# Performance work log

Hardware: AMD Instinct MI355X
Metric: run time of the kernel (lower is better)

Reference implementation:

```python
import jax, jax.numpy as jnp
import numpy as np

B = 1024       # batch of graphs
NUM = 512      # predicates / nodes per graph
D = 64         # embedding_dim
H = 64         # hidden_dim
E = 4096       # edges per graph (shared structure across batch)
MAIN_NUM = 10  # softmax segment [0, MAIN_NUM); sigmoid on the rest


def setup_inputs() -> dict:
    key = jax.random.key(0)
    ks = jax.random.split(key, 8)
    x = jax.random.uniform(ks[0], (B, NUM), dtype=jnp.float32)
    embedding = jax.random.normal(ks[1], (NUM, D), dtype=jnp.float32) * 0.1
    W1 = jax.random.normal(ks[2], (D, H), dtype=jnp.float32) * (1.0 / np.sqrt(D))
    b1 = jnp.zeros((H,), jnp.float32)
    W2 = jax.random.normal(ks[3], (H, H), dtype=jnp.float32) * (1.0 / np.sqrt(H))
    b2 = jnp.zeros((H,), jnp.float32)
    W3 = jax.random.normal(ks[4], (H, 1), dtype=jnp.float32) * (1.0 / np.sqrt(H))
    b3 = jnp.zeros((1,), jnp.float32)
    edge_row = jax.random.randint(ks[5], (E,), 0, NUM, dtype=jnp.int32)
    edge_col = jax.random.randint(ks[6], (E,), 0, NUM, dtype=jnp.int32)
    return {"x": x, "embedding": embedding, "W1": W1, "b1": b1,
            "W2": W2, "b2": b2, "W3": W3, "b3": b3,
            "edge_row": edge_row, "edge_col": edge_col}


def _gcn_layer(h, W, b, row, col, norm):
    # h: [B, NUM, in]; GCNConv = linear -> D^{-1/2} A D^{-1/2} aggregate -> +bias
    hW = jnp.einsum('bni,io->bno', h, W)                 # [B, NUM, out]
    msg = hW[:, row, :] * norm[None, :, None]            # [B, E, out]
    agg = jnp.zeros_like(hW).at[:, col, :].add(msg)      # scatter to targets
    return agg + b


def reference(x, embedding, W1, b1, W2, b2, W3, b3, edge_row, edge_col):
    num = x.shape[1]
    # symmetric GCN normalization (add_self_loops=False, unit edge weights)
    deg = jnp.zeros((num,), x.dtype).at[edge_col].add(1.0)
    dinv = jnp.where(deg > 0, jax.lax.rsqrt(jnp.maximum(deg, 1.0)), 0.0)
    norm = dinv[edge_row] * dinv[edge_col]               # [E]

    h = x[..., None] * embedding                         # [B, NUM, D]
    h = jax.nn.relu(_gcn_layer(h, W1, b1, edge_row, edge_col, norm))
    h = jax.nn.relu(_gcn_layer(h, W2, b2, edge_row, edge_col, norm))
    logits = _gcn_layer(h, W3, b3, edge_row, edge_col, norm)[..., 0]  # [B, NUM]

    # convert_to_confidence: softmax over multiclass segment, sigmoid elsewhere
    phi_sm = jax.nn.softmax(logits[:, :MAIN_NUM], axis=1)
    phi_sg = jax.nn.sigmoid(logits[:, MAIN_NUM:])
    return jnp.concatenate([phi_sm, phi_sg], axis=1)
```

## Files before the change

### kernel.cpp

```cpp
#include <hip/hip_runtime.h>
#include <stdint.h>

#define NB    1024
#define NUM   512
#define HD    64
#define NE    4096
#define NEP   4608
#define MAIN  10
#define HBS   72

typedef _Float16 hlf;
typedef __attribute__((ext_vector_type(2))) _Float16 hlf2;
typedef __attribute__((ext_vector_type(8))) _Float16 hlf8;
typedef __attribute__((ext_vector_type(4))) float f32x4;

__device__ __forceinline__ unsigned short f2h(float f) {
    hlf v = (hlf)f;
    return __builtin_bit_cast(unsigned short, v);
}

__global__ __launch_bounds__(512) void prep_all(
    const int* __restrict__ erow, const int* __restrict__ ecol,
    const float* __restrict__ emb, const float* __restrict__ W1,
    const float* __restrict__ W2,
    int* __restrict__ rsptr, int* __restrict__ colmap, int* __restrict__ epk,
    short* __restrict__ E1, short* __restrict__ W2T)
{
    const int t = threadIdx.x;
    if (blockIdx.x != 0) {
        int g = (blockIdx.x - 1) * 512 + t;
        if (g < NUM * HD) {
            int node = g >> 6, dim = g & 63;
            float acc = 0.0f;
            #pragma unroll
            for (int k = 0; k < HD; ++k) acc += emb[node * HD + k] * W1[k * HD + dim];
            E1[g] = (short)f2h(acc);
        } else if (g < NUM * HD + HD * HD) {
            int j = g - NUM * HD;
            int dout = j >> 6, din = j & 63;
            W2T[j] = (short)f2h(W2[din * HD + dout]);
        }
        return;
    }

    __shared__ int   sdeg[NUM];
    __shared__ int   aux[NUM];
    __shared__ float sdv[NUM];
    __shared__ int   rnk[NUM];
    __shared__ int   rdg[NUM];
    __shared__ int   wsum[8];

    const int lane = t & 63, wv = t >> 6;

    sdeg[t] = 0; aux[t] = 0;
    __syncthreads();
    for (int e = t; e < NE; e += 512) atomicAdd(&sdeg[ecol[e]], 1);
    __syncthreads();
    const int deg  = sdeg[t];
    const int pdeg = (deg + 1) & ~1;
    const int dbin = deg < NUM ? deg : NUM - 1;
    sdv[t] = deg > 0 ? rsqrtf((float)deg) : 0.0f;
    atomicAdd(&aux[dbin], 1);
    __syncthreads();
    {
        int v = aux[t];
        #pragma unroll
        for (int ofs = 1; ofs < 64; ofs <<= 1) {
            int sh = __shfl_up(v, ofs, 64);
            if (lane >= ofs) v += sh;
        }
        if (lane == 63) wsum[wv] = v;
        __syncthreads();
        if (t == 0) {
            int s = 0;
            #pragma unroll
            for (int w = 0; w < 8; ++w) { int tmp = wsum[w]; wsum[w] = s; s += tmp; }
        }
        __syncthreads();
        int inc = v + wsum[wv];
        aux[t]  = inc;
        __syncthreads();
        sdeg[t] = (t == 0) ? 0 : aux[t - 1];
        __syncthreads();
    }
    {
        int r = atomicAdd(&sdeg[dbin], 1);
        rnk[t] = r;
        rdg[r] = pdeg;
        colmap[r] = t;
    }
    __syncthreads();
    {
        int dv = rdg[t], v = dv;
        #pragma unroll
        for (int ofs = 1; ofs < 64; ofs <<= 1) {
            int sh = __shfl_up(v, ofs, 64);
            if (lane >= ofs) v += sh;
        }
        if (lane == 63) wsum[wv] = v;
        __syncthreads();
        if (t == 0) {
            int s = 0;
            #pragma unroll
            for (int w = 0; w < 8; ++w) { int tmp = wsum[w]; wsum[w] = s; s += tmp; }
        }
        __syncthreads();
        int inc  = v + wsum[wv];
        int excl = inc - dv;
        rsptr[t] = excl;
        if (t == NUM - 1) rsptr[NUM] = inc;
        aux[t] = excl;
        __syncthreads();
    }
    sdeg[t] = aux[rnk[t]];
    __syncthreads();
    for (int i = t; i < NEP; i += 512) epk[i] = 0;
    __syncthreads();
    for (int e = t; e < NE; e += 512) {
        int c = ecol[e], rr = erow[e];
        int p = atomicAdd(&sdeg[c], 1);
        unsigned ns = (unsigned)f2h(sdv[rr] * sdv[c]);
        epk[p] = (rr << 23) | (int)ns;
    }
}

__global__ __launch_bounds__(1024, 4) void gcn_body(
    const float* __restrict__ x, const hlf* __restrict__ E1,
    const hlf* __restrict__ W2T,
    const float* __restrict__ b1, const float* __restrict__ b2,
    const float* __restrict__ W3, const float* __restrict__ b3,
    const int* __restrict__ rsptrg, const int* __restrict__ colmap,
    const int* __restrict__ epkg,
    float* __restrict__ out)
{
    __shared__ hlf HA[NUM * HD];
    __shared__ hlf HB[NUM * HBS];
    __shared__ int eps[NEP + 8];
    __shared__ int sptr[513];
    __shared__ float sred[2];

    float* tv   = (float*)HB;
    float* slog = ((float*)HB) + NUM;

    const int t     = threadIdx.x;
    const int b     = blockIdx.x;
    const int lane  = t & 63;
    const int wave  = t >> 6;
    const int q     = lane >> 4;
    const int l15   = lane & 15;
    const int grp   = lane >> 3;
    const int dbase = (lane & 7) * 8;

    {
        const int4* g4 = (const int4*)epkg;
        *(int4*)&eps[t * 4] = g4[t];
        if (t < 128) *(int4*)&eps[4096 + t * 4] = g4[1024 + t];
        if (t < 8)   eps[NEP + t] = 0;
    }
    if (t < 513) sptr[t] = rsptrg[t];

    #pragma unroll
    for (int p = 0; p < 4; ++p) {
        int i = t + p * 1024;
        int r = i >> 3, d8 = (i & 7) * 8;
        float xr = x[b * NUM + r];
        hlf  xh = (hlf)xr;
        hlf8 e  = *(const hlf8*)&E1[r * HD + d8];
        hlf8 o;
        #pragma unroll
        for (int j = 0; j < 8; ++j) o[j] = e[j] * xh;
        *(hlf8*)&HA[r * HD + d8] = o;
    }

    float b1v[8], b2v[8], w3v[8];
    {
        f32x4 u0 = *(const f32x4*)&b1[dbase], u1 = *(const f32x4*)&b1[dbase + 4];
        f32x4 v0 = *(const f32x4*)&b2[dbase], v1 = *(const f32x4*)&b2[dbase + 4];
        f32x4 w0 = *(const f32x4*)&W3[dbase], w1 = *(const f32x4*)&W3[dbase + 4];
        #pragma unroll
        for (int j = 0; j < 4; ++j) {
            b1v[j] = u0[j]; b1v[j + 4] = u1[j];
            b2v[j] = v0[j]; b2v[j + 4] = v1[j];
            w3v[j] = w0[j]; w3v[j + 4] = w1[j];
        }
    }
    const char* HAb = (const char*)HA + dbase * 2;
    __syncthreads();

#define LDROW(d, pe) d = *(const uint4*)(HAb + ((unsigned)(pe) >> 16));
#define MACROW(hv, pe) {                                                      \
        const hlf nh = __builtin_bit_cast(hlf2, (unsigned)(pe))[0];           \
        const hlf2 p0 = __builtin_bit_cast(hlf2, (hv).x);                     \
        const hlf2 p1 = __builtin_bit_cast(hlf2, (hv).y);                     \
        const hlf2 p2 = __builtin_bit_cast(hlf2, (hv).z);                     \
        const hlf2 p3 = __builtin_bit_cast(hlf2, (hv).w);                     \
        a[0] = fmaf((float)p0[0], (float)nh, a[0]);                           \
        a[1] = fmaf((float)p0[1], (float)nh, a[1]);                           \
        a[2] = fmaf((float)p1[0], (float)nh, a[2]);                           \
        a[3] = fmaf((float)p1[1], (float)nh, a[3]);                           \
        a[4] = fmaf((float)p2[0], (float)nh, a[4]);                           \
        a[5] = fmaf((float)p2[1], (float)nh, a[5]);                           \
        a[6] = fmaf((float)p3[0], (float)nh, a[6]);                           \
        a[7] = fmaf((float)p3[1], (float)nh, a[7]); }

#define SPMM_PIPE(E0, E1v)                                                    \
    int e = E0;                                                               \
    int2 qa0 = *(const int2*)&eps[e], qb0 = *(const int2*)&eps[e + 2];        \
    uint4 u0, u1, u2, u3;                                                     \
    LDROW(u0, qa0.x) LDROW(u1, qa0.y) LDROW(u2, qb0.x) LDROW(u3, qb0.y)       \
    for (; e + 4 < E1v; e += 4) {                                             \
        int2 qa1 = *(const int2*)&eps[e + 4];                                 \
        int2 qb1 = *(const int2*)&eps[e + 6];                                 \
        uint4 w0, w1, w2, w3;                                                 \
        LDROW(w0, qa1.x) LDROW(w1, qa1.y) LDROW(w2, qb1.x) LDROW(w3, qb1.y)   \
        MACROW(u0, qa0.x) MACROW(u1, qa0.y)                                   \
        MACROW(u2, qb0.x) MACROW(u3, qb0.y)                                   \
        qa0 = qa1; qb0 = qb1; u0 = w0; u1 = w1; u2 = w2; u3 = w3;             \
    }                                                                         \
    if (e < E1v)     { MACROW(u0, qa0.x) MACROW(u1, qa0.y) }                  \
    if (e + 2 < E1v) { MACROW(u2, qb0.x) MACROW(u3, qb0.y) }

    #pragma unroll 1
    for (int set = 0; set < 4; ++set) {
        int wv8 = ((set & 1) ? (15 - wave) : wave) * 8;
        int r  = set * 128 + wv8 + grp;
        int e0 = sptr[r], e1 = sptr[r + 1];
        int c  = colmap[r];
        float a[8];
        #pragma unroll
        for (int j = 0; j < 8; ++j) a[j] = 0.0f;
        { SPMM_PIPE(e0, e1) }
        uint4 ov;
        ov.x = __builtin_bit_cast(unsigned, __builtin_amdgcn_cvt_pkrtz(
                   fmaxf(a[0] + b1v[0], 0.0f), fmaxf(a[1] + b1v[1], 0.0f)));
        ov.y = __builtin_bit_cast(unsigned, __builtin_amdgcn_cvt_pkrtz(
                   fmaxf(a[2] + b1v[2], 0.0f), fmaxf(a[3] + b1v[3], 0.0f)));
        ov.z = __builtin_bit_cast(unsigned, __builtin_amdgcn_cvt_pkrtz(
                   fmaxf(a[4] + b1v[4], 0.0f), fmaxf(a[5] + b1v[5], 0.0f)));
        ov.w = __builtin_bit_cast(unsigned, __builtin_amdgcn_cvt_pkrtz(
                   fmaxf(a[6] + b1v[6], 0.0f), fmaxf(a[7] + b1v[7], 0.0f)));
        *(uint4*)&HB[c * HBS + dbase] = ov;
    }
    __syncthreads();

    {
        hlf8 bfr[2][4];
        #pragma unroll
        for (int ks = 0; ks < 2; ++ks)
            #pragma unroll
            for (int nt = 0; nt < 4; ++nt)
                bfr[ks][nt] = *(const hlf8*)&W2T[(nt * 16 + l15) * HD + ks * 32 + q * 8];
        f32x4 acc[2][4];
        #pragma unroll
        for (int mt = 0; mt < 2; ++mt)
            #pragma unroll
            for (int nt = 0; nt < 4; ++nt) acc[mt][nt] = (f32x4){0.f, 0.f, 0.f, 0.f};
        const int mbase = wave * 32;
        #pragma unroll
        for (int mt = 0; mt < 2; ++mt)
            #pragma unroll
            for (int ks = 0; ks < 2; ++ks) {
                hlf8 af = *(const hlf8*)&HB[(mbase + mt * 16 + l15) * HBS
                                            + ks * 32 + q * 8];
                #pragma unroll
                for (int nt = 0; nt < 4; ++nt)
                    acc[mt][nt] = __builtin_amdgcn_mfma_f32_16x16x32_f16(
                        af, bfr[ks][nt], acc[mt][nt], 0, 0, 0);
            }
        #pragma unroll
        for (int mt = 0; mt < 2; ++mt)
            #pragma unroll
            for (int nt = 0; nt < 4; ++nt)
                #pragma unroll
                for (int i = 0; i < 4; ++i)
                    HA[(mbase + mt * 16 + q * 4 + i) * HD + nt * 16 + l15] =
                        (hlf)acc[mt][nt][i];
    }
    __syncthreads();

    #pragma unroll 1
    for (int set = 0; set < 4; ++set) {
        int wv8 = ((set & 1) ? (15 - wave) : wave) * 8;
        int r  = set * 128 + wv8 + grp;
        int e0 = sptr[r], e1 = sptr[r + 1];
        int c  = colmap[r];
        float a[8];
        #pragma unroll
        for (int j = 0; j < 8; ++j) a[j] = 0.0f;
        { SPMM_PIPE(e0, e1) }
        float v = 0.0f;
        #pragma unroll
        for (int j = 0; j < 8; ++j)
            v += fmaxf(a[j] + b2v[j], 0.0f) * w3v[j];
        v += __shfl_xor(v, 1, 64);
        v += __shfl_xor(v, 2, 64);
        v += __shfl_xor(v, 4, 64);
        if ((lane & 7) == 0) tv[c] = v;
    }
    __syncthreads();

    {
        int rk = t >> 1, hh = t & 1;
        int e0 = sptr[rk], e1 = sptr[rk + 1];
        int mid = (e0 + e1) >> 1;
        int ea = hh ? mid : e0;
        int eb = hh ? e1 : mid;
        float acc = 0.0f;
        for (int e = ea; e < eb; ++e) {
            unsigned pe = (unsigned)eps[e];
            float nf = (float)__builtin_bit_cast(hlf2, pe)[0];
            acc = fmaf(nf, *(const float*)((const char*)tv + (pe >> 21)), acc);
        }
        acc += __shfl_xor(acc, 1, 64);
        if (!hh) slog[colmap[rk]] = acc + b3[0];
    }
    __syncthreads();

    if (t < 64) {
        float v = (t < MAIN) ? slog[t] : -1e30f;
        float m = v;
        m = fmaxf(m, __shfl_xor(m, 1, 64));
        m = fmaxf(m, __shfl_xor(m, 2, 64));
        m = fmaxf(m, __shfl_xor(m, 4, 64));
        m = fmaxf(m, __shfl_xor(m, 8, 64));
        float ev = (t < MAIN) ? __expf(v - m) : 0.0f;
        ev += __shfl_xor(ev, 1, 64);
        ev += __shfl_xor(ev, 2, 64);
        ev += __shfl_xor(ev, 4, 64);
        ev += __shfl_xor(ev, 8, 64);
        if (t == 0) { sred[0] = m; sred[1] = ev; }
    }
    __syncthreads();

    if (t < NUM) {
        float l = slog[t];
        float o = (t < MAIN) ? __expf(l - sred[0]) / sred[1]
                             : 1.0f / (1.0f + __expf(-l));
        out[b * NUM + t] = o;
    }
#undef LDROW
#undef MACROW
#undef SPMM_PIPE
}

extern "C" void kernel_launch(void* const* d_in, const int* in_sizes, int n_in,
                              void* d_out, int out_size, void* d_ws, size_t ws_size,
                              hipStream_t stream) {
    const float* x    = (const float*)d_in[0];
    const float* emb  = (const float*)d_in[1];
    const float* W1   = (const float*)d_in[2];
    const float* b1   = (const float*)d_in[3];
    const float* W2   = (const float*)d_in[4];
    const float* b2   = (const float*)d_in[5];
    const float* W3   = (const float*)d_in[6];
    const float* b3   = (const float*)d_in[7];
    const int*   erow = (const int*)d_in[8];
    const int*   ecol = (const int*)d_in[9];

    char* ws = (char*)d_ws;
    int*   rsptr  = (int*)ws;
    int*   colmap = (int*)(ws + 2176);
    int*   epk    = (int*)(ws + 4224);
    short* E1     = (short*)(ws + 22656);
    short* W2T    = (short*)(ws + 88192);

    prep_all<<<73, 512, 0, stream>>>(erow, ecol, emb, W1, W2,
                                     rsptr, colmap, epk, E1, W2T);
    gcn_body<<<NB, 1024, 0, stream>>>(x, (const hlf*)E1, (const hlf*)W2T,
                                      b1, b2, W3, b3,
                                      rsptr, colmap, epk, (float*)d_out);
}
```

Measured before the change: 158.5 us.

## Shrink LDS to a single H buffer and read edge list from global

```diff
diff --git a/kernel.cpp b/kernel.cpp
--- a/kernel.cpp
+++ b/kernel.cpp
@@ -7,7 +7,6 @@
 #define NE    4096
 #define NEP   4608
 #define MAIN  10
-#define HBS   72
 
 typedef _Float16 hlf;
 typedef __attribute__((ext_vector_type(2))) _Float16 hlf2;
@@ -124,23 +123,21 @@
     }
 }
 
-__global__ __launch_bounds__(1024, 4) void gcn_body(
+__global__ __launch_bounds__(1024, 8) void gcn_body(
     const float* __restrict__ x, const hlf* __restrict__ E1,
     const hlf* __restrict__ W2T,
     const float* __restrict__ b1, const float* __restrict__ b2,
     const float* __restrict__ W3, const float* __restrict__ b3,
-    const int* __restrict__ rsptrg, const int* __restrict__ colmap,
+    const int* __restrict__ rsptrg, const int* __restrict__ colmapg,
     const int* __restrict__ epkg,
     float* __restrict__ out)
 {
-    __shared__ hlf HA[NUM * HD];
-    __shared__ hlf HB[NUM * HBS];
-    __shared__ int eps[NEP + 8];
-    __shared__ int sptr[513];
+    __shared__ hlf   H[NUM * HD];
+    __shared__ int   sptr[513];
+    __shared__ int   cmap[NUM];
+    __shared__ float tv[NUM];
+    __shared__ float slog[NUM];
     __shared__ float sred[2];
-
-    float* tv   = (float*)HB;
-    float* slog = ((float*)HB) + NUM;
 
     const int t     = threadIdx.x;
     const int b     = blockIdx.x;
@@ -151,13 +148,8 @@
     const int grp   = lane >> 3;
     const int dbase = (lane & 7) * 8;
 
-    {
-        const int4* g4 = (const int4*)epkg;
-        *(int4*)&eps[t * 4] = g4[t];
-        if (t < 128) *(int4*)&eps[4096 + t * 4] = g4[1024 + t];
-        if (t < 8)   eps[NEP + t] = 0;
-    }
     if (t < 513) sptr[t] = rsptrg[t];
+    if (t < NUM) cmap[t] = colmapg[t];
 
     #pragma unroll
     for (int p = 0; p < 4; ++p) {
@@ -169,129 +161,130 @@
         hlf8 o;
         #pragma unroll
         for (int j = 0; j < 8; ++j) o[j] = e[j] * xh;
-        *(hlf8*)&HA[r * HD + d8] = o;
-    }
-
-    float b1v[8], b2v[8], w3v[8];
-    {
-        f32x4 u0 = *(const f32x4*)&b1[dbase], u1 = *(const f32x4*)&b1[dbase + 4];
-        f32x4 v0 = *(const f32x4*)&b2[dbase], v1 = *(const f32x4*)&b2[dbase + 4];
-        f32x4 w0 = *(const f32x4*)&W3[dbase], w1 = *(const f32x4*)&W3[dbase + 4];
-        #pragma unroll
-        for (int j = 0; j < 4; ++j) {
-            b1v[j] = u0[j]; b1v[j + 4] = u1[j];
-            b2v[j] = v0[j]; b2v[j + 4] = v1[j];
-            w3v[j] = w0[j]; w3v[j + 4] = w1[j];
-        }
-    }
-    const char* HAb = (const char*)HA + dbase * 2;
-    __syncthreads();
-
-#define LDROW(d, pe) d = *(const uint4*)(HAb + ((unsigned)(pe) >> 16));
-#define MACROW(hv, pe) {                                                      \
+        *(hlf8*)&H[r * HD + d8] = o;
+    }
+    const char* Hb = (const char*)H + dbase * 2;
+    __syncthreads();
+
+#define MACROW(acc, hv, pe) {                                                 \
         const hlf nh = __builtin_bit_cast(hlf2, (unsigned)(pe))[0];           \
         const hlf2 p0 = __builtin_bit_cast(hlf2, (hv).x);                     \
         const hlf2 p1 = __builtin_bit_cast(hlf2, (hv).y);                     \
         const hlf2 p2 = __builtin_bit_cast(hlf2, (hv).z);                     \
         const hlf2 p3 = __builtin_bit_cast(hlf2, (hv).w);                     \
-        a[0] = fmaf((float)p0[0], (float)nh, a[0]);                           \
-        a[1] = fmaf((float)p0[1], (float)nh, a[1]);                           \
-        a[2] = fmaf((float)p1[0], (float)nh, a[2]);                           \
-        a[3] = fmaf((float)p1[1], (float)nh, a[3]);                           \
-        a[4] = fmaf((float)p2[0], (float)nh, a[4]);                           \
-        a[5] = fmaf((float)p2[1], (float)nh, a[5]);                           \
-        a[6] = fmaf((float)p3[0], (float)nh, a[6]);                           \
-        a[7] = fmaf((float)p3[1], (float)nh, a[7]); }
-
-#define SPMM_PIPE(E0, E1v)                                                    \
-    int e = E0;                                                               \
-    int2 qa0 = *(const int2*)&eps[e], qb0 = *(const int2*)&eps[e + 2];        \
-    uint4 u0, u1, u2, u3;                                                     \
-    LDROW(u0, qa0.x) LDROW(u1, qa0.y) LDROW(u2, qb0.x) LDROW(u3, qb0.y)       \
-    for (; e + 4 < E1v; e += 4) {                                             \
-        int2 qa1 = *(const int2*)&eps[e + 4];                                 \
-        int2 qb1 = *(const int2*)&eps[e + 6];                                 \
-        uint4 w0, w1, w2, w3;                                                 \
-        LDROW(w0, qa1.x) LDROW(w1, qa1.y) LDROW(w2, qb1.x) LDROW(w3, qb1.y)   \
-        MACROW(u0, qa0.x) MACROW(u1, qa0.y)                                   \
-        MACROW(u2, qb0.x) MACROW(u3, qb0.y)                                   \
-        qa0 = qa1; qb0 = qb1; u0 = w0; u1 = w1; u2 = w2; u3 = w3;             \
-    }                                                                         \
-    if (e < E1v)     { MACROW(u0, qa0.x) MACROW(u1, qa0.y) }                  \
-    if (e + 2 < E1v) { MACROW(u2, qb0.x) MACROW(u3, qb0.y) }
+        acc[0] = fmaf((float)p0[0], (float)nh, acc[0]);                       \
+        acc[1] = fmaf((float)p0[1], (float)nh, acc[1]);                       \
+        acc[2] = fmaf((float)p1[0], (float)nh, acc[2]);                       \
+        acc[3] = fmaf((float)p1[1], (float)nh, acc[3]);                       \
+        acc[4] = fmaf((float)p2[0], (float)nh, acc[4]);                       \
+        acc[5] = fmaf((float)p2[1], (float)nh, acc[5]);                       \
+        acc[6] = fmaf((float)p3[0], (float)nh, acc[6]);                       \
+        acc[7] = fmaf((float)p3[1], (float)nh, acc[7]); }
+
+    {
+        uint4 hv[4];
+        #pragma unroll 1
+        for (int set = 0; set < 4; ++set) {
+            int r  = set * 128 + wave * 8 + grp;
+            int e0 = sptr[r], e1 = sptr[r + 1];
+            float a[8];
+            #pragma unroll
+            for (int j = 0; j < 8; ++j) a[j] = 0.0f;
+            for (int e = e0; e < e1; e += 2) {
+                int2 qa = *(const int2*)&epkg[e];
+                uint4 c0 = *(const uint4*)(Hb + ((unsigned)qa.x >> 16));
+                uint4 c1 = *(const uint4*)(Hb + ((unsigned)qa.y >> 16));
+                MACROW(a, c0, qa.x) MACROW(a, c1, qa.y)
+            }
+            f32x4 u0 = *(const f32x4*)&b1[dbase];
+            f32x4 u1 = *(const f32x4*)&b1[dbase + 4];
+            hv[set].x = __builtin_bit_cast(unsigned, __builtin_amdgcn_cvt_pkrtz(
+                            fmaxf(a[0] + u0[0], 0.0f), fmaxf(a[1] + u0[1], 0.0f)));
+            hv[set].y = __builtin_bit_cast(unsigned, __builtin_amdgcn_cvt_pkrtz(
+                            fmaxf(a[2] + u0[2], 0.0f), fmaxf(a[3] + u0[3], 0.0f)));
+            hv[set].z = __builtin_bit_cast(unsigned, __builtin_amdgcn_cvt_pkrtz(
+                            fmaxf(a[4] + u1[0], 0.0f), fmaxf(a[5] + u1[1], 0.0f)));
+            hv[set].w = __builtin_bit_cast(unsigned, __builtin_amdgcn_cvt_pkrtz(
+                            fmaxf(a[6] + u1[2], 0.0f), fmaxf(a[7] + u1[3], 0.0f)));
+        }
+        __syncthreads();
+        #pragma unroll
+        for (int set = 0; set < 4; ++set) {
+            int r = set * 128 + wave * 8 + grp;
+            *(uint4*)&H[cmap[r] * HD + dbase] = hv[set];
+        }
+    }
+    __syncthreads();
+
+    {
+        uint2 gk[2][4];
+        #pragma unroll 1
+        for (int mm = 0; mm < 2; ++mm) {
+            int m = wave * 32 + mm * 16 + l15;
+            hlf8 a0 = *(const hlf8*)&H[m * HD + q * 8];
+            hlf8 a1 = *(const hlf8*)&H[m * HD + 32 + q * 8];
+            #pragma unroll
+            for (int nt = 0; nt < 4; ++nt) {
+                hlf8 w0 = *(const hlf8*)&W2T[(nt * 16 + l15) * HD + q * 8];
+                hlf8 w1 = *(const hlf8*)&W2T[(nt * 16 + l15) * HD + 32 + q * 8];
+                f32x4 acc = (f32x4){0.f, 0.f, 0.f, 0.f};
+                acc = __builtin_amdgcn_mfma_f32_16x16x32_f16(a0, w0, acc, 0, 0, 0);
+                acc = __builtin_amdgcn_mfma_f32_16x16x32_f16(a1, w1, acc, 0, 0, 0);
+                gk[mm][nt].x = __builtin_bit_cast(unsigned,
+                                   __builtin_amdgcn_cvt_pkrtz(acc[0], acc[1]));
+                gk[mm][nt].y = __builtin_bit_cast(unsigned,
+                                   __builtin_amdgcn_cvt_pkrtz(acc[2], acc[3]));
+            }
+        }
+        __syncthreads();
+        #pragma unroll
+        for (int mm = 0; mm < 2; ++mm)
+            #pragma unroll
+            for (int nt = 0; nt < 4; ++nt) {
+                int mrow = wave * 32 + mm * 16 + q * 4;
+                hlf2 lo = __builtin_bit_cast(hlf2, gk[mm][nt].x);
+                hlf2 hi = __builtin_bit_cast(hlf2, gk[mm][nt].y);
+                H[(mrow + 0) * HD + nt * 16 + l15] = lo[0];
+                H[(mrow + 1) * HD + nt * 16 + l15] = lo[1];
+                H[(mrow + 2) * HD + nt * 16 + l15] = hi[0];
+                H[(mrow + 3) * HD + nt * 16 + l15] = hi[1];
+            }
+    }
+    __syncthreads();
 
     #pragma unroll 1
     for (int set = 0; set < 4; ++set) {
-        int wv8 = ((set & 1) ? (15 - wave) : wave) * 8;
-        int r  = set * 128 + wv8 + grp;
+        int r  = set * 128 + wave * 8 + grp;
         int e0 = sptr[r], e1 = sptr[r + 1];
-        int c  = colmap[r];
+        int c  = cmap[r];
         float a[8];
         #pragma unroll
         for (int j = 0; j < 8; ++j) a[j] = 0.0f;
-        { SPMM_PIPE(e0, e1) }
-        uint4 ov;
-        ov.x = __builtin_bit_cast(unsigned, __builtin_amdgcn_cvt_pkrtz(
-                   fmaxf(a[0] + b1v[0], 0.0f), fmaxf(a[1] + b1v[1], 0.0f)));
-        ov.y = __builtin_bit_cast(unsigned, __builtin_amdgcn_cvt_pkrtz(
-                   fmaxf(a[2] + b1v[2], 0.0f), fmaxf(a[3] + b1v[3], 0.0f)));
-        ov.z = __builtin_bit_cast(unsigned, __builtin_amdgcn_cvt_pkrtz(
-                   fmaxf(a[4] + b1v[4], 0.0f), fmaxf(a[5] + b1v[5], 0.0f)));
-        ov.w = __builtin_bit_cast(unsigned, __builtin_amdgcn_cvt_pkrtz(
-                   fmaxf(a[6] + b1v[6], 0.0f), fmaxf(a[7] + b1v[7], 0.0f)));
-        *(uint4*)&HB[c * HBS + dbase] = ov;
-    }
-    __syncthreads();
-
-    {
-        hlf8 bfr[2][4];
-        #pragma unroll
-        for (int ks = 0; ks < 2; ++ks)
-            #pragma unroll
-            for (int nt = 0; nt < 4; ++nt)
-                bfr[ks][nt] = *(const hlf8*)&W2T[(nt * 16 + l15) * HD + ks * 32 + q * 8];
-        f32x4 acc[2][4];
-        #pragma unroll
-        for (int mt = 0; mt < 2; ++mt)
-            #pragma unroll
-            for (int nt = 0; nt < 4; ++nt) acc[mt][nt] = (f32x4){0.f, 0.f, 0.f, 0.f};
-        const int mbase = wave * 32;
-        #pragma unroll
-        for (int mt = 0; mt < 2; ++mt)
-            #pragma unroll
-            for (int ks = 0; ks < 2; ++ks) {
-                hlf8 af = *(const hlf8*)&HB[(mbase + mt * 16 + l15) * HBS
-                                            + ks * 32 + q * 8];
-                #pragma unroll
-                for (int nt = 0; nt < 4; ++nt)
-                    acc[mt][nt] = __builtin_amdgcn_mfma_f32_16x16x32_f16(
-                        af, bfr[ks][nt], acc[mt][nt], 0, 0, 0);
-            }
-        #pragma unroll
-        for (int mt = 0; mt < 2; ++mt)
-            #pragma unroll
-            for (int nt = 0; nt < 4; ++nt)
-                #pragma unroll
-                for (int i = 0; i < 4; ++i)
-                    HA[(mbase + mt * 16 + q * 4 + i) * HD + nt * 16 + l15] =
-                        (hlf)acc[mt][nt][i];
-    }
-    __syncthreads();
-
-    #pragma unroll 1
-    for (int set = 0; set < 4; ++set) {
-        int wv8 = ((set & 1) ? (15 - wave) : wave) * 8;
-        int r  = set * 128 + wv8 + grp;
-        int e0 = sptr[r], e1 = sptr[r + 1];
-        int c  = colmap[r];
-        float a[8];
-        #pragma unroll
-        for (int j = 0; j < 8; ++j) a[j] = 0.0f;
-        { SPMM_PIPE(e0, e1) }
+        int e = e0;
+        for (; e + 4 <= e1; e += 4) {
+            int2 qa = *(const int2*)&epkg[e];
+            int2 qb = *(const int2*)&epkg[e + 2];
+            uint4 c0 = *(const uint4*)(Hb + ((unsigned)qa.x >> 16));
+            uint4 c1 = *(const uint4*)(Hb + ((unsigned)qa.y >> 16));
+            uint4 c2 = *(const uint4*)(Hb + ((unsigned)qb.x >> 16));
+            uint4 c3 = *(const uint4*)(Hb + ((unsigned)qb.y >> 16));
+            MACROW(a, c0, qa.x) MACROW(a, c1, qa.y)
+            MACROW(a, c2, qb.x) MACROW(a, c3, qb.y)
+        }
+        if (e < e1) {
+            int2 qa = *(const int2*)&epkg[e];
+            uint4 c0 = *(const uint4*)(Hb + ((unsigned)qa.x >> 16));
+            uint4 c1 = *(const uint4*)(Hb + ((unsigned)qa.y >> 16));
+            MACROW(a, c0, qa.x) MACROW(a, c1, qa.y)
+        }
+        f32x4 v0 = *(const f32x4*)&b2[dbase], v1 = *(const f32x4*)&b2[dbase + 4];
+        f32x4 w0 = *(const f32x4*)&W3[dbase], w1 = *(const f32x4*)&W3[dbase + 4];
         float v = 0.0f;
         #pragma unroll
-        for (int j = 0; j < 8; ++j)
-            v += fmaxf(a[j] + b2v[j], 0.0f) * w3v[j];
+        for (int j = 0; j < 4; ++j) {
+            v += fmaxf(a[j] + v0[j], 0.0f) * w0[j];
+            v += fmaxf(a[j + 4] + v1[j], 0.0f) * w1[j];
+        }
         v += __shfl_xor(v, 1, 64);
         v += __shfl_xor(v, 2, 64);
         v += __shfl_xor(v, 4, 64);
@@ -307,12 +300,12 @@
         int eb = hh ? e1 : mid;
         float acc = 0.0f;
         for (int e = ea; e < eb; ++e) {
-            unsigned pe = (unsigned)eps[e];
+            unsigned pe = (unsigned)epkg[e];
             float nf = (float)__builtin_bit_cast(hlf2, pe)[0];
             acc = fmaf(nf, *(const float*)((const char*)tv + (pe >> 21)), acc);
         }
         acc += __shfl_xor(acc, 1, 64);
-        if (!hh) slog[colmap[rk]] = acc + b3[0];
+        if (!hh) slog[cmap[rk]] = acc + b3[0];
     }
     __syncthreads();
 
@@ -338,9 +331,7 @@
                              : 1.0f / (1.0f + __expf(-l));
         out[b * NUM + t] = o;
     }
-#undef LDROW
 #undef MACROW
-#undef SPMM_PIPE
 }
 
 extern "C" void kernel_launch(void* const* d_in, const int* in_sizes, int n_in,
```

Result: slower. 182.6 us (+15.2%).
